# Kernel optimization log

Measured on AMD Instinct MI355X. Metric: run time of the kernel, lower is better.

## Reference

```python
import jax, jax.numpy as jnp
import numpy as np

N_NODES = 100000
N_EDGES = 1600000
IN_F = 128
HID = 128
OUT_F = 40


def _gcn_conv(x, W, b, src, dst):
    # PyG GCNConv: h = x @ W; out[dst] += norm * h[src]; out += b
    n = x.shape[0]
    h = x @ W  # [N, out_channels]
    deg = jnp.zeros((n,), h.dtype).at[dst].add(jnp.ones((dst.shape[0],), h.dtype))
    dinv = jnp.where(deg > 0, jax.lax.rsqrt(deg), 0.0)  # deg^{-1/2}
    norm = dinv[src] * dinv[dst]  # [E+N]
    msg = h[src] * norm[:, None]  # [E+N, out_channels] gather
    out = jnp.zeros_like(h).at[dst].add(msg)  # scatter-add at targets
    if b is not None:
        out = out + b
    return out


def setup_inputs() -> dict:
    key = jax.random.key(0)
    k_x, k_e, k1, k2, k3, kb1, kb2 = jax.random.split(key, 7)
    x = jax.random.normal(k_x, (N_NODES, IN_F), dtype=jnp.float32)
    edge_index = jax.random.randint(k_e, (2, N_EDGES), 0, N_NODES, dtype=jnp.int64)
    s_in = 1.0 / np.sqrt(IN_F)
    s_h = 1.0 / np.sqrt(HID)
    W_in = jax.random.normal(k1, (IN_F, HID), dtype=jnp.float32) * s_in
    b_in = jnp.zeros((HID,), dtype=jnp.float32)
    W_mid = jax.random.normal(k2, (HID, HID), dtype=jnp.float32) * s_h
    b_mid = jnp.zeros((HID,), dtype=jnp.float32)
    W_out = jax.random.normal(k3, (HID, OUT_F), dtype=jnp.float32) * s_h
    return {"x": x, "edge_index": edge_index, "W_in": W_in, "b_in": b_in,
            "W_mid": W_mid, "b_mid": b_mid, "W_out": W_out}


def reference(x, edge_index, W_in, b_in, W_mid, b_mid, W_out):
    n = x.shape[0]
    loops = jnp.arange(n, dtype=edge_index.dtype)
    src = jnp.concatenate([edge_index[0], loops])  # add self-loops
    dst = jnp.concatenate([edge_index[1], loops])
    h = jax.nn.relu(_gcn_conv(x, W_in, b_in, src, dst))
    h = jax.nn.relu(_gcn_conv(h, W_mid, b_mid, src, dst))
    h = _gcn_conv(h, W_out, None, src, dst)  # out_conv: bias=False
    return jax.nn.log_softmax(h, axis=1)
```

## Files before the change

kernel.cpp:

```cpp
#include <hip/hip_runtime.h>
#include <math.h>

#define N_NODES 100000
#define N_EDGES 1600000
#define NBUCK 391
#define BSTRIDE 4608

typedef __attribute__((ext_vector_type(8))) _Float16 h8v;
typedef __attribute__((ext_vector_type(4))) float f32x4;


__launch_bounds__(256)
__global__ void k_bpart(const int* __restrict__ srcv, const int* __restrict__ dstv,
                        int* __restrict__ bcnt, unsigned int* __restrict__ ebuf) {
    __shared__ int hist[NBUCK];
    __shared__ int cur[NBUCK];
    const int tid = threadIdx.x;
    for (int t = tid; t < NBUCK; t += 256) hist[t] = 0;
    __syncthreads();
    const int base = blockIdx.x * 4096;
#pragma unroll
    for (int i = 0; i < 16; i++) {
        int e = base + i * 256 + tid;
        if (e < N_EDGES) atomicAdd(&hist[dstv[e] >> 8], 1);
    }
    __syncthreads();
    for (int t = tid; t < NBUCK; t += 256)
        if (hist[t]) cur[t] = t * BSTRIDE + atomicAdd(&bcnt[t], hist[t]);
    __syncthreads();
#pragma unroll
    for (int i = 0; i < 16; i++) {
        int e = base + i * 256 + tid;
        if (e < N_EDGES) {
            int d = dstv[e];
            int p = atomicAdd(&cur[d >> 8], 1);
            ebuf[p] = ((unsigned int)srcv[e] << 8) | (unsigned int)(d & 255);
        }
    }
}

__launch_bounds__(256)
__global__ void k_bucket(const unsigned int* __restrict__ ebuf, const int* __restrict__ bcnt,
                         int2* __restrict__ rowse, float* __restrict__ dinv,
                         int* __restrict__ colidx) {
    __shared__ int cnt[256];
    __shared__ int s[256];
    __shared__ int cur[256];
    const int tid = threadIdx.x;
    const int b = blockIdx.x;
    const int e0 = b * BSTRIDE;
    const int e1 = e0 + bcnt[b];
    cnt[tid] = 0;
    __syncthreads();
    for (int e = e0 + tid; e < e1; e += 256) atomicAdd(&cnt[ebuf[e] & 255u], 1);
    __syncthreads();
    int v = cnt[tid];
    int x = v;
    s[tid] = x;
    __syncthreads();
    for (int d = 1; d < 256; d <<= 1) {
        int t = (tid >= d) ? s[tid - d] : 0;
        __syncthreads();
        x += t;
        s[tid] = x;
        __syncthreads();
    }
    int start = e0 + x - v;
    int node = b * 256 + tid;
    if (node < N_NODES) {
        rowse[node] = make_int2(start, start + v);
        dinv[node] = rsqrtf((float)(v + 1));
    }
    cur[tid] = start;
    __syncthreads();
    for (int e = e0 + tid; e < e1; e += 256) {
        unsigned int sd = ebuf[e];
        int pos = atomicAdd(&cur[sd & 255u], 1);
        colidx[pos] = (int)(sd >> 8);
    }
}

__global__ void k_zrows(_Float16* __restrict__ bufA, _Float16* __restrict__ zbuf) {
    int t = threadIdx.x;
    if (t < 128) bufA[(size_t)N_NODES * 128 + t] = (_Float16)0.f;
    if (t < 64)  zbuf[(size_t)N_NODES * 64 + t] = (_Float16)0.f;
}


__global__ void k_wprep_all(const float* __restrict__ W1, const float* __restrict__ W2,
                            const float* __restrict__ W3, _Float16* __restrict__ Wt) {
    int idx = blockIdx.x * blockDim.x + threadIdx.x;
    if (idx >= 304 * 128) return;
    int n = idx / 128, k = idx % 128;
    const float* W;
    int ncols, nloc;
    _Float16 *ph, *pl;
    if (n < 128)      { W = W1; ncols = 128; nloc = n;       ph = Wt;                 pl = Wt + 128 * 128; }
    else if (n < 256) { W = W2; ncols = 128; nloc = n - 128; ph = Wt + 2 * 128 * 128; pl = Wt + 3 * 128 * 128; }
    else              { W = W3; ncols = 40;  nloc = n - 256; ph = Wt + 4 * 128 * 128; pl = Wt + 4 * 128 * 128 + 48 * 128; }
    float v = (nloc < ncols) ? W[k * ncols + nloc] : 0.f;
    _Float16 hi = (_Float16)v;
    _Float16 lo = (_Float16)(v - (float)hi);
    ph[nloc * 128 + k] = hi;
    pl[nloc * 128 + k] = lo;
}


#define GEMM_GRID 625
#define NTILES 3125

__launch_bounds__(256, 2)
__global__ void k_gemm128_f32(const float* __restrict__ Af,
                              const _Float16* __restrict__ Wthi, const _Float16* __restrict__ Wtlo,
                              const float* __restrict__ dinv, _Float16* __restrict__ out) {
    const int lane = threadIdx.x & 63;
    const int wi = threadIdx.x >> 6;
    const int nb = wi * 32;
    const int nn = lane & 15;
    const int kq = (lane >> 4) * 8;
    const int quad = lane >> 4;

    h8v bh[4][2], bl[4][2];
#pragma unroll
    for (int c = 0; c < 4; c++)
#pragma unroll
        for (int t = 0; t < 2; t++) {
            int off = (nb + t * 16 + nn) * 128 + c * 32 + kq;
            bh[c][t] = *(const h8v*)(Wthi + off);
            bl[c][t] = *(const h8v*)(Wtlo + off);
        }

    for (int rt = blockIdx.x; rt < NTILES; rt += GEMM_GRID) {
        const int r0 = rt * 32;
        f32x4 acc[2][2] = {};
#pragma unroll
        for (int c = 0; c < 4; c++) {
            h8v a[2];
#pragma unroll
            for (int m = 0; m < 2; m++) {
                const float* p = Af + (size_t)(r0 + m * 16 + nn) * 128 + c * 32 + kq;
                float4 p0 = *(const float4*)p;
                float4 p1 = *(const float4*)(p + 4);
                h8v av = {(_Float16)p0.x, (_Float16)p0.y, (_Float16)p0.z, (_Float16)p0.w,
                          (_Float16)p1.x, (_Float16)p1.y, (_Float16)p1.z, (_Float16)p1.w};
                a[m] = av;
            }
#pragma unroll
            for (int m = 0; m < 2; m++)
#pragma unroll
                for (int t = 0; t < 2; t++) {
                    acc[m][t] = __builtin_amdgcn_mfma_f32_16x16x32_f16(a[m], bh[c][t], acc[m][t], 0, 0, 0);
                    acc[m][t] = __builtin_amdgcn_mfma_f32_16x16x32_f16(a[m], bl[c][t], acc[m][t], 0, 0, 0);
                }
        }
#pragma unroll
        for (int m = 0; m < 2; m++)
#pragma unroll
            for (int reg = 0; reg < 4; reg++) {
                int r = r0 + m * 16 + quad * 4 + reg;
                float dv = dinv[r];
#pragma unroll
                for (int t = 0; t < 2; t++)
                    out[(size_t)r * 128 + nb + t * 16 + nn] = (_Float16)(acc[m][t][reg] * dv);
            }
    }
}

__launch_bounds__(256, 2)
__global__ void k_gemm128(const _Float16* __restrict__ A,
                          const _Float16* __restrict__ Wthi, const _Float16* __restrict__ Wtlo,
                          const float* __restrict__ dinv, _Float16* __restrict__ out) {
    const int lane = threadIdx.x & 63;
    const int wi = threadIdx.x >> 6;
    const int nb = wi * 32;
    const int nn = lane & 15;
    const int kq = (lane >> 4) * 8;
    const int quad = lane >> 4;

    h8v bh[4][2], bl[4][2];
#pragma unroll
    for (int c = 0; c < 4; c++)
#pragma unroll
        for (int t = 0; t < 2; t++) {
            int off = (nb + t * 16 + nn) * 128 + c * 32 + kq;
            bh[c][t] = *(const h8v*)(Wthi + off);
            bl[c][t] = *(const h8v*)(Wtlo + off);
        }

    for (int rt = blockIdx.x; rt < NTILES; rt += GEMM_GRID) {
        const int r0 = rt * 32;
        f32x4 acc[2][2] = {};
#pragma unroll
        for (int c = 0; c < 4; c++) {
            h8v a[2];
#pragma unroll
            for (int m = 0; m < 2; m++)
                a[m] = *(const h8v*)(A + (size_t)(r0 + m * 16 + nn) * 128 + c * 32 + kq);
#pragma unroll
            for (int m = 0; m < 2; m++)
#pragma unroll
                for (int t = 0; t < 2; t++) {
                    acc[m][t] = __builtin_amdgcn_mfma_f32_16x16x32_f16(a[m], bh[c][t], acc[m][t], 0, 0, 0);
                    acc[m][t] = __builtin_amdgcn_mfma_f32_16x16x32_f16(a[m], bl[c][t], acc[m][t], 0, 0, 0);
                }
        }
#pragma unroll
        for (int m = 0; m < 2; m++)
#pragma unroll
            for (int reg = 0; reg < 4; reg++) {
                int r = r0 + m * 16 + quad * 4 + reg;
                float dv = dinv[r];
#pragma unroll
                for (int t = 0; t < 2; t++)
                    out[(size_t)r * 128 + nb + t * 16 + nn] = (_Float16)(acc[m][t][reg] * dv);
            }
    }
}

#define G40_GRID 160

__launch_bounds__(256, 2)
__global__ void k_gemm40(const _Float16* __restrict__ A,
                         const _Float16* __restrict__ Wthi, const _Float16* __restrict__ Wtlo,
                         const float* __restrict__ dinv, _Float16* __restrict__ out) {
    const int lane = threadIdx.x & 63;
    const int wi = threadIdx.x >> 6;
    const int nn = lane & 15;
    const int kq = (lane >> 4) * 8;
    const int quad = lane >> 4;

    h8v bh[4][3], bl[4][3];
#pragma unroll
    for (int c = 0; c < 4; c++)
#pragma unroll
        for (int t = 0; t < 3; t++) {
            int off = (t * 16 + nn) * 128 + c * 32 + kq;
            bh[c][t] = *(const h8v*)(Wthi + off);
            bl[c][t] = *(const h8v*)(Wtlo + off);
        }

    for (int rt = blockIdx.x * 4 + wi; rt < NTILES; rt += G40_GRID * 4) {
        const int r0 = rt * 32;
        f32x4 acc[2][3] = {};
#pragma unroll
        for (int c = 0; c < 4; c++) {
            h8v a[2];
#pragma unroll
            for (int m = 0; m < 2; m++)
                a[m] = *(const h8v*)(A + (size_t)(r0 + m * 16 + nn) * 128 + c * 32 + kq);
#pragma unroll
            for (int m = 0; m < 2; m++)
#pragma unroll
                for (int t = 0; t < 3; t++) {
                    acc[m][t] = __builtin_amdgcn_mfma_f32_16x16x32_f16(a[m], bh[c][t], acc[m][t], 0, 0, 0);
                    acc[m][t] = __builtin_amdgcn_mfma_f32_16x16x32_f16(a[m], bl[c][t], acc[m][t], 0, 0, 0);
                }
        }
#pragma unroll
        for (int m = 0; m < 2; m++)
#pragma unroll
            for (int reg = 0; reg < 4; reg++) {
                int r = r0 + m * 16 + quad * 4 + reg;
                float dv = dinv[r];
#pragma unroll
                for (int t = 0; t < 3; t++)
                    out[(size_t)r * 64 + t * 16 + nn] = (_Float16)(acc[m][t][reg] * dv);
            }
    }
}


__launch_bounds__(256)
__global__ void k_agg4(const _Float16* __restrict__ hp, const int2* __restrict__ rowse,
                       const int* __restrict__ colidx, const float* __restrict__ bias,
                       _Float16* __restrict__ outp) {
    const int lane = threadIdx.x & 63;
    const int wid = (blockIdx.x * blockDim.x + threadIdx.x) >> 6;
    const int rs = lane >> 4;
    const int cp = lane & 15;
    const int r = wid * 4 + rs;

    const int2 se = rowse[r];
    const int deg = se.y - se.x;
    int m = deg;
    m = max(m, __shfl_xor(m, 16));
    m = max(m, __shfl_xor(m, 32));

    const _Float16* hpc = hp + cp * 8;
    h8v acc = {};
    for (int it = 0; it < m; it += 4) {
        int i0 = se.x + it;
        int s0 = colidx[i0];
        int s1 = colidx[i0 + 1];
        int s2 = colidx[i0 + 2];
        int s3 = colidx[i0 + 3];
        s0 = (it < deg) ? s0 : N_NODES;
        s1 = (it + 1 < deg) ? s1 : N_NODES;
        s2 = (it + 2 < deg) ? s2 : N_NODES;
        s3 = (it + 3 < deg) ? s3 : N_NODES;
        h8v v0 = *(const h8v*)(hpc + (size_t)s0 * 128);
        h8v v1 = *(const h8v*)(hpc + (size_t)s1 * 128);
        h8v v2 = *(const h8v*)(hpc + (size_t)s2 * 128);
        h8v v3 = *(const h8v*)(hpc + (size_t)s3 * 128);
        acc += v0;
        acc += v1;
        acc += v2;
        acc += v3;
    }

    h8v sv = *(const h8v*)(hpc + (size_t)r * 128);
    float dv = rsqrtf((float)(deg + 1));
    const float* bp = bias + cp * 8;
    float4 b0 = *(const float4*)bp;
    float4 b1 = *(const float4*)(bp + 4);
    float bb[8] = {b0.x, b0.y, b0.z, b0.w, b1.x, b1.y, b1.z, b1.w};
    h8v o;
#pragma unroll
    for (int j = 0; j < 8; j++) {
        float s = (float)acc[j] + (float)sv[j];
        o[j] = (_Float16)fmaxf(fmaf(dv, s, bb[j]), 0.f);
    }
    *(h8v*)(outp + (size_t)r * 128 + cp * 8) = o;
}


__launch_bounds__(256)
__global__ void k_agg_out(const _Float16* __restrict__ hp, const int2* __restrict__ rowse,
                          const int* __restrict__ colidx, float* __restrict__ out) {
    const int lane = threadIdx.x & 63;
    const int wid = (blockIdx.x * blockDim.x + threadIdx.x) >> 6;
    const int rs = lane >> 3;
    const int cp = lane & 7;
    const int r = wid * 8 + rs;

    const int2 se = rowse[r];
    const int deg = se.y - se.x;
    int m = deg;
    m = max(m, __shfl_xor(m, 8));
    m = max(m, __shfl_xor(m, 16));
    m = max(m, __shfl_xor(m, 32));

    const _Float16* hpc = hp + cp * 8;
    h8v acc = {};
    for (int it = 0; it < m; it += 4) {
        int i0 = se.x + it;
        int s0 = colidx[i0];
        int s1 = colidx[i0 + 1];
        int s2 = colidx[i0 + 2];
        int s3 = colidx[i0 + 3];
        s0 = (it < deg) ? s0 : N_NODES;
        s1 = (it + 1 < deg) ? s1 : N_NODES;
        s2 = (it + 2 < deg) ? s2 : N_NODES;
        s3 = (it + 3 < deg) ? s3 : N_NODES;
        h8v v0 = *(const h8v*)(hpc + (size_t)s0 * 64);
        h8v v1 = *(const h8v*)(hpc + (size_t)s1 * 64);
        h8v v2 = *(const h8v*)(hpc + (size_t)s2 * 64);
        h8v v3 = *(const h8v*)(hpc + (size_t)s3 * 64);
        acc += v0;
        acc += v1;
        acc += v2;
        acc += v3;
    }

    h8v sv = *(const h8v*)(hpc + (size_t)r * 64);
    float dv = rsqrtf((float)(deg + 1));
    float z[8];
#pragma unroll
    for (int j = 0; j < 8; j++) z[j] = dv * ((float)acc[j] + (float)sv[j]);

    const bool act = cp < 5;
    float pm = -INFINITY;
    if (act) {
#pragma unroll
        for (int j = 0; j < 8; j++) pm = fmaxf(pm, z[j]);
    }
    pm = fmaxf(pm, __shfl_xor(pm, 1));
    pm = fmaxf(pm, __shfl_xor(pm, 2));
    pm = fmaxf(pm, __shfl_xor(pm, 4));
    float pe = 0.f;
    if (act) {
#pragma unroll
        for (int j = 0; j < 8; j++) pe += __expf(z[j] - pm);
    }
    pe += __shfl_xor(pe, 1);
    pe += __shfl_xor(pe, 2);
    pe += __shfl_xor(pe, 4);
    float lse = __logf(pe);
    if (act) {
        float* po = out + (size_t)r * 40 + cp * 8;
        float4 o0 = make_float4(z[0] - pm - lse, z[1] - pm - lse, z[2] - pm - lse, z[3] - pm - lse);
        float4 o1 = make_float4(z[4] - pm - lse, z[5] - pm - lse, z[6] - pm - lse, z[7] - pm - lse);
        *(float4*)po = o0;
        *(float4*)(po + 4) = o1;
    }
}


extern "C" void kernel_launch(void* const* d_in, const int* in_sizes, int n_in,
                              void* d_out, int out_size, void* d_ws, size_t ws_size,
                              hipStream_t stream) {
    const float* x     = (const float*)d_in[0];
    const int*   ei    = (const int*)d_in[1];
    const float* W_in  = (const float*)d_in[2];
    const float* b_in  = (const float*)d_in[3];
    const float* W_mid = (const float*)d_in[4];
    const float* b_mid = (const float*)d_in[5];
    const float* W_out = (const float*)d_in[6];
    float* out = (float*)d_out;

    const int* srcv = ei;
    const int* dstv = ei + N_EDGES;

    char* w = (char*)d_ws;
    float* dinv   = (float*)(w);
    int2* rowse   = (int2*)(w + (1ull << 19));
    int* bcnt     = (int*)(w + 1507328);
    int* colidx   = (int*)(w + (2ull << 20));
    unsigned int* ebuf = (unsigned int*)(w + (10ull << 20));
    _Float16* Wt  = (_Float16*)(w + (18ull << 20));
    _Float16* bufA = (_Float16*)(w + (19ull << 20));
    _Float16* bufB = (_Float16*)(w + (45ull << 20));
    _Float16* zbuf = (_Float16*)(w + (71ull << 20));

    _Float16* W1h = Wt;
    _Float16* W1l = Wt + 128 * 128;
    _Float16* W2h = Wt + 2 * 128 * 128;
    _Float16* W2l = Wt + 3 * 128 * 128;
    _Float16* W3h = Wt + 4 * 128 * 128;
    _Float16* W3l = Wt + 4 * 128 * 128 + 48 * 128;

    const int NB_PART = (N_EDGES + 4095) / 4096;

    hipMemsetAsync(bcnt, 0, NBUCK * sizeof(int), stream);
    k_zrows<<<1, 256, 0, stream>>>(bufA, zbuf);
    k_bpart<<<NB_PART, 256, 0, stream>>>(srcv, dstv, bcnt, ebuf);
    k_bucket<<<NBUCK, 256, 0, stream>>>(ebuf, bcnt, rowse, dinv, colidx);

    k_wprep_all<<<(304 * 128 + 255) / 256, 256, 0, stream>>>(W_in, W_mid, W_out, Wt);

    const int AGG4_BLOCKS = N_NODES / 16;
    const int AGGO_BLOCKS = N_NODES / 32;

    k_gemm128_f32<<<GEMM_GRID, 256, 0, stream>>>(x, W1h, W1l, dinv, bufA);
    k_agg4<<<AGG4_BLOCKS, 256, 0, stream>>>(bufA, rowse, colidx, b_in, bufB);
    k_gemm128<<<GEMM_GRID, 256, 0, stream>>>(bufB, W2h, W2l, dinv, bufA);
    k_agg4<<<AGG4_BLOCKS, 256, 0, stream>>>(bufA, rowse, colidx, b_mid, bufB);
    k_gemm40<<<G40_GRID, 256, 0, stream>>>(bufB, W3h, W3l, dinv, zbuf);
    k_agg_out<<<AGGO_BLOCKS, 256, 0, stream>>>(zbuf, rowse, colidx, out);
}
```

Baseline: 366.9 us.

## Store hidden features column-blocked so aggregation gathers from cache-resident slices

Hidden feature buffers move from row-major [N,128] to eight column blocks of 16 halves per node, each block laid out as [N+1,16]. The GEMMs read and write in this blocked layout. The 128-wide aggregation kernel now runs one column block per grid slice, so each block's gather touches a 3.2MB slice that can stay in cache instead of the full 25MB table. The cost is that edge indices and row ranges are re-read eight times, and each gather is only 32 bytes per lane pair. Column-index loads are also marked nontemporal.

```diff
diff --git a/kernel.cpp b/kernel.cpp
--- a/kernel.cpp
+++ b/kernel.cpp
@@ -8,6 +8,7 @@
 
 typedef __attribute__((ext_vector_type(8))) _Float16 h8v;
 typedef __attribute__((ext_vector_type(4))) float f32x4;
+
 
 
 __launch_bounds__(256)
@@ -82,7 +83,9 @@
 
 __global__ void k_zrows(_Float16* __restrict__ bufA, _Float16* __restrict__ zbuf) {
     int t = threadIdx.x;
-    if (t < 128) bufA[(size_t)N_NODES * 128 + t] = (_Float16)0.f;
+    if (t < 128) {
+        bufA[((size_t)(t >> 4) * (N_NODES + 1) + N_NODES) * 16 + (t & 15)] = (_Float16)0.f;
+    }
     if (t < 64)  zbuf[(size_t)N_NODES * 64 + t] = (_Float16)0.f;
 }
 
@@ -160,8 +163,10 @@
                 int r = r0 + m * 16 + quad * 4 + reg;
                 float dv = dinv[r];
 #pragma unroll
-                for (int t = 0; t < 2; t++)
-                    out[(size_t)r * 128 + nb + t * 16 + nn] = (_Float16)(acc[m][t][reg] * dv);
+                for (int t = 0; t < 2; t++) {
+                    int blk = (nb >> 4) + t;
+                    out[((size_t)blk * (N_NODES + 1) + r) * 16 + nn] = (_Float16)(acc[m][t][reg] * dv);
+                }
             }
     }
 }
@@ -194,8 +199,10 @@
         for (int c = 0; c < 4; c++) {
             h8v a[2];
 #pragma unroll
-            for (int m = 0; m < 2; m++)
-                a[m] = *(const h8v*)(A + (size_t)(r0 + m * 16 + nn) * 128 + c * 32 + kq);
+            for (int m = 0; m < 2; m++) {
+                int blk = 2 * c + (kq >> 4);
+                a[m] = *(const h8v*)(A + ((size_t)blk * (N_NODES + 1) + (r0 + m * 16 + nn)) * 16 + (kq & 8));
+            }
 #pragma unroll
             for (int m = 0; m < 2; m++)
 #pragma unroll
@@ -211,8 +218,10 @@
                 int r = r0 + m * 16 + quad * 4 + reg;
                 float dv = dinv[r];
 #pragma unroll
-                for (int t = 0; t < 2; t++)
-                    out[(size_t)r * 128 + nb + t * 16 + nn] = (_Float16)(acc[m][t][reg] * dv);
+                for (int t = 0; t < 2; t++) {
+                    int blk = (nb >> 4) + t;
+                    out[((size_t)blk * (N_NODES + 1) + r) * 16 + nn] = (_Float16)(acc[m][t][reg] * dv);
+                }
             }
     }
 }
@@ -246,8 +255,10 @@
         for (int c = 0; c < 4; c++) {
             h8v a[2];
 #pragma unroll
-            for (int m = 0; m < 2; m++)
-                a[m] = *(const h8v*)(A + (size_t)(r0 + m * 16 + nn) * 128 + c * 32 + kq);
+            for (int m = 0; m < 2; m++) {
+                int blk = 2 * c + (kq >> 4);
+                a[m] = *(const h8v*)(A + ((size_t)blk * (N_NODES + 1) + (r0 + m * 16 + nn)) * 16 + (kq & 8));
+            }
 #pragma unroll
             for (int m = 0; m < 2; m++)
 #pragma unroll
@@ -275,52 +286,60 @@
                        const int* __restrict__ colidx, const float* __restrict__ bias,
                        _Float16* __restrict__ outp) {
     const int lane = threadIdx.x & 63;
-    const int wid = (blockIdx.x * blockDim.x + threadIdx.x) >> 6;
-    const int rs = lane >> 4;
-    const int cp = lane & 15;
-    const int r = wid * 4 + rs;
-
-    const int2 se = rowse[r];
+    const int wi = threadIdx.x >> 6;
+    const int c = blockIdx.x & 7;
+    const int tile = blockIdx.x >> 3;
+    const int rs = lane >> 1;
+    const int cp = lane & 1;
+    const int r = tile * 128 + wi * 32 + rs;
+
+    int2 se = make_int2(0, 0);
+    if (r < N_NODES) se = rowse[r];
     const int deg = se.y - se.x;
     int m = deg;
+    m = max(m, __shfl_xor(m, 2));
+    m = max(m, __shfl_xor(m, 4));
+    m = max(m, __shfl_xor(m, 8));
     m = max(m, __shfl_xor(m, 16));
     m = max(m, __shfl_xor(m, 32));
 
-    const _Float16* hpc = hp + cp * 8;
+    const _Float16* hpc = hp + ((size_t)c * (N_NODES + 1)) * 16 + cp * 8;
     h8v acc = {};
     for (int it = 0; it < m; it += 4) {
         int i0 = se.x + it;
-        int s0 = colidx[i0];
-        int s1 = colidx[i0 + 1];
-        int s2 = colidx[i0 + 2];
-        int s3 = colidx[i0 + 3];
+        int s0 = __builtin_nontemporal_load(colidx + i0);
+        int s1 = __builtin_nontemporal_load(colidx + i0 + 1);
+        int s2 = __builtin_nontemporal_load(colidx + i0 + 2);
+        int s3 = __builtin_nontemporal_load(colidx + i0 + 3);
         s0 = (it < deg) ? s0 : N_NODES;
         s1 = (it + 1 < deg) ? s1 : N_NODES;
         s2 = (it + 2 < deg) ? s2 : N_NODES;
         s3 = (it + 3 < deg) ? s3 : N_NODES;
-        h8v v0 = *(const h8v*)(hpc + (size_t)s0 * 128);
-        h8v v1 = *(const h8v*)(hpc + (size_t)s1 * 128);
-        h8v v2 = *(const h8v*)(hpc + (size_t)s2 * 128);
-        h8v v3 = *(const h8v*)(hpc + (size_t)s3 * 128);
+        h8v v0 = *(const h8v*)(hpc + (size_t)s0 * 16);
+        h8v v1 = *(const h8v*)(hpc + (size_t)s1 * 16);
+        h8v v2 = *(const h8v*)(hpc + (size_t)s2 * 16);
+        h8v v3 = *(const h8v*)(hpc + (size_t)s3 * 16);
         acc += v0;
         acc += v1;
         acc += v2;
         acc += v3;
     }
 
-    h8v sv = *(const h8v*)(hpc + (size_t)r * 128);
-    float dv = rsqrtf((float)(deg + 1));
-    const float* bp = bias + cp * 8;
-    float4 b0 = *(const float4*)bp;
-    float4 b1 = *(const float4*)(bp + 4);
-    float bb[8] = {b0.x, b0.y, b0.z, b0.w, b1.x, b1.y, b1.z, b1.w};
-    h8v o;
-#pragma unroll
-    for (int j = 0; j < 8; j++) {
-        float s = (float)acc[j] + (float)sv[j];
-        o[j] = (_Float16)fmaxf(fmaf(dv, s, bb[j]), 0.f);
-    }
-    *(h8v*)(outp + (size_t)r * 128 + cp * 8) = o;
+    if (r < N_NODES) {
+        h8v sv = *(const h8v*)(hpc + (size_t)r * 16);
+        float dv = rsqrtf((float)(deg + 1));
+        const float* bp = bias + c * 16 + cp * 8;
+        float4 b0 = *(const float4*)bp;
+        float4 b1 = *(const float4*)(bp + 4);
+        float bb[8] = {b0.x, b0.y, b0.z, b0.w, b1.x, b1.y, b1.z, b1.w};
+        h8v o;
+#pragma unroll
+        for (int j = 0; j < 8; j++) {
+            float sx = (float)acc[j] + (float)sv[j];
+            o[j] = (_Float16)fmaxf(fmaf(dv, sx, bb[j]), 0.f);
+        }
+        *(h8v*)(outp + ((size_t)c * (N_NODES + 1) + r) * 16 + cp * 8) = o;
+    }
 }
 
 
@@ -438,7 +457,7 @@
 
     k_wprep_all<<<(304 * 128 + 255) / 256, 256, 0, stream>>>(W_in, W_mid, W_out, Wt);
 
-    const int AGG4_BLOCKS = N_NODES / 16;
+    const int AGG4_BLOCKS = 8 * ((N_NODES + 127) / 128);
     const int AGGO_BLOCKS = N_NODES / 32;
 
     k_gemm128_f32<<<GEMM_GRID, 256, 0, stream>>>(x, W1h, W1l, dinv, bufA);
```

New measurement: 505.4 us. 37.7% more time.

## Fuse first GEMM, edge partition and weight prep into one prep kernel

Applied to the files above, without the earlier changes.

Merges the first-layer GEMM (x@W1), the edge bucket partition, the W2/W3 fp16 split prep and the zero-row init into a single heterogeneous launch, with the GEMM converting W1 on the fly. Because the GEMM no longer waits for dinv, the dinv row scaling moves into k_bucket, which rescales bufA in place after building the CSR. This removes several launches and lets the dense GEMM overlap with the irregular partition work. In exchange bufA is read and written an extra time, and each GEMM block recomputes the W1 hi/lo split from strided global reads.

```diff
diff --git a/kernel.cpp b/kernel.cpp
--- a/kernel.cpp
+++ b/kernel.cpp
@@ -8,17 +8,115 @@
 
 typedef __attribute__((ext_vector_type(8))) _Float16 h8v;
 typedef __attribute__((ext_vector_type(4))) float f32x4;
-
-
-__launch_bounds__(256)
-__global__ void k_bpart(const int* __restrict__ srcv, const int* __restrict__ dstv,
-                        int* __restrict__ bcnt, unsigned int* __restrict__ ebuf) {
+typedef __attribute__((ext_vector_type(2))) int i32x2;
+
+#define GEMM_GRID 625
+#define NTILES 3125
+
+
+__global__ void k_prep(const int* __restrict__ srcv, const int* __restrict__ dstv,
+                       int* __restrict__ bcnt, unsigned int* __restrict__ ebuf,
+                       const float* __restrict__ x, const float* __restrict__ W1,
+                       const float* __restrict__ W2, const float* __restrict__ W3,
+                       _Float16* __restrict__ Wt,
+                       _Float16* __restrict__ bufA, _Float16* __restrict__ bufB,
+                       _Float16* __restrict__ zbuf) {
+    const int tid = threadIdx.x;
+    const int bid = blockIdx.x;
+
+    if (bid < 625) {
+        const int lane = tid & 63;
+        const int wi = tid >> 6;
+        const int nb = wi * 32;
+        const int nn = lane & 15;
+        const int quad = lane >> 4;
+        const int kq = quad * 8;
+
+        h8v bh[4][2], bl[4][2];
+#pragma unroll
+        for (int c = 0; c < 4; c++)
+#pragma unroll
+            for (int t = 0; t < 2; t++) {
+#pragma unroll
+                for (int j = 0; j < 8; j++) {
+                    float w = W1[(c * 32 + kq + j) * 128 + nb + t * 16 + nn];
+                    _Float16 hi = (_Float16)w;
+                    bh[c][t][j] = hi;
+                    bl[c][t][j] = (_Float16)(w - (float)hi);
+                }
+            }
+
+        for (int rt = bid; rt < NTILES; rt += GEMM_GRID) {
+            const int r0 = rt * 32;
+            f32x4 acc[2][2] = {};
+#pragma unroll
+            for (int c = 0; c < 4; c++) {
+                h8v a[2];
+#pragma unroll
+                for (int m = 0; m < 2; m++) {
+                    const float* p = x + (size_t)(r0 + m * 16 + nn) * 128 + c * 32 + kq;
+                    float4 p0 = *(const float4*)p;
+                    float4 p1 = *(const float4*)(p + 4);
+                    h8v av = {(_Float16)p0.x, (_Float16)p0.y, (_Float16)p0.z, (_Float16)p0.w,
+                              (_Float16)p1.x, (_Float16)p1.y, (_Float16)p1.z, (_Float16)p1.w};
+                    a[m] = av;
+                }
+#pragma unroll
+                for (int m = 0; m < 2; m++)
+#pragma unroll
+                    for (int t = 0; t < 2; t++) {
+                        acc[m][t] = __builtin_amdgcn_mfma_f32_16x16x32_f16(a[m], bh[c][t], acc[m][t], 0, 0, 0);
+                        acc[m][t] = __builtin_amdgcn_mfma_f32_16x16x32_f16(a[m], bl[c][t], acc[m][t], 0, 0, 0);
+                    }
+            }
+#pragma unroll
+            for (int m = 0; m < 2; m++)
+#pragma unroll
+                for (int reg = 0; reg < 4; reg++) {
+                    int r = r0 + m * 16 + quad * 4 + reg;
+#pragma unroll
+                    for (int t = 0; t < 2; t++)
+                        bufA[(size_t)r * 128 + nb + t * 16 + nn] = (_Float16)acc[m][t][reg];
+                }
+        }
+        return;
+    }
+
+    if (bid >= 1016) {
+        if (bid == 1104) {
+            if (tid < 128) {
+                bufA[(size_t)N_NODES * 128 + tid] = (_Float16)0.f;
+                bufB[(size_t)N_NODES * 128 + tid] = (_Float16)0.f;
+            }
+            if (tid < 64)  zbuf[(size_t)N_NODES * 64 + tid] = (_Float16)0.f;
+            return;
+        }
+        int idx = (bid - 1016) * 256 + tid;
+        if (idx >= 176 * 128) return;
+        int n = idx / 128, k = idx % 128;
+        _Float16 *ph, *pl;
+        float v;
+        if (n < 128) {
+            v = W2[k * 128 + n];
+            ph = Wt + 2 * 128 * 128; pl = Wt + 3 * 128 * 128;
+        } else {
+            int nloc = n - 128;
+            v = (nloc < 40) ? W3[k * 40 + nloc] : 0.f;
+            ph = Wt + 4 * 128 * 128; pl = Wt + 4 * 128 * 128 + 48 * 128;
+            n = nloc;
+        }
+        _Float16 hi = (_Float16)v;
+        _Float16 lo = (_Float16)(v - (float)hi);
+        ph[n * 128 + k] = hi;
+        pl[n * 128 + k] = lo;
+        return;
+    }
+
     __shared__ int hist[NBUCK];
     __shared__ int cur[NBUCK];
-    const int tid = threadIdx.x;
     for (int t = tid; t < NBUCK; t += 256) hist[t] = 0;
     __syncthreads();
-    const int base = blockIdx.x * 4096;
+    const int base = (bid - 625) * 4096;
 #pragma unroll
     for (int i = 0; i < 16; i++) {
         int e = base + i * 256 + tid;
@@ -39,13 +137,15 @@
     }
 }
 
+
 __launch_bounds__(256)
 __global__ void k_bucket(const unsigned int* __restrict__ ebuf, const int* __restrict__ bcnt,
-                         int2* __restrict__ rowse, float* __restrict__ dinv,
-                         int* __restrict__ colidx) {
+                         i32x2* __restrict__ rowse, float* __restrict__ dinv,
+                         int* __restrict__ colidx, _Float16* __restrict__ bufA) {
     __shared__ int cnt[256];
     __shared__ int s[256];
     __shared__ int cur[256];
+    __shared__ float sdv[256];
     const int tid = threadIdx.x;
     const int b = blockIdx.x;
     const int e0 = b * BSTRIDE;
@@ -67,9 +167,14 @@
     }
     int start = e0 + x - v;
     int node = b * 256 + tid;
+    float dvv = rsqrtf((float)(v + 1));
+    sdv[tid] = dvv;
     if (node < N_NODES) {
-        rowse[node] = make_int2(start, start + v);
-        dinv[node] = rsqrtf((float)(v + 1));
+        i32x2 se;
+        se.x = start;
+        se.y = start + v;
+        rowse[node] = se;
+        dinv[node] = dvv;
     }
     cur[tid] = start;
     __syncthreads();
@@ -78,200 +183,28 @@
         int pos = atomicAdd(&cur[sd & 255u], 1);
         colidx[pos] = (int)(sd >> 8);
     }
-}
-
-__global__ void k_zrows(_Float16* __restrict__ bufA, _Float16* __restrict__ zbuf) {
-    int t = threadIdx.x;
-    if (t < 128) bufA[(size_t)N_NODES * 128 + t] = (_Float16)0.f;
-    if (t < 64)  zbuf[(size_t)N_NODES * 64 + t] = (_Float16)0.f;
-}
-
-
-__global__ void k_wprep_all(const float* __restrict__ W1, const float* __restrict__ W2,
-                            const float* __restrict__ W3, _Float16* __restrict__ Wt) {
-    int idx = blockIdx.x * blockDim.x + threadIdx.x;
-    if (idx >= 304 * 128) return;
-    int n = idx / 128, k = idx % 128;
-    const float* W;
-    int ncols, nloc;
-    _Float16 *ph, *pl;
-    if (n < 128)      { W = W1; ncols = 128; nloc = n;       ph = Wt;                 pl = Wt + 128 * 128; }
-    else if (n < 256) { W = W2; ncols = 128; nloc = n - 128; ph = Wt + 2 * 128 * 128; pl = Wt + 3 * 128 * 128; }
-    else              { W = W3; ncols = 40;  nloc = n - 256; ph = Wt + 4 * 128 * 128; pl = Wt + 4 * 128 * 128 + 48 * 128; }
-    float v = (nloc < ncols) ? W[k * ncols + nloc] : 0.f;
-    _Float16 hi = (_Float16)v;
-    _Float16 lo = (_Float16)(v - (float)hi);
-    ph[nloc * 128 + k] = hi;
-    pl[nloc * 128 + k] = lo;
-}
-
-
-#define GEMM_GRID 625
-#define NTILES 3125
-
-__launch_bounds__(256, 2)
-__global__ void k_gemm128_f32(const float* __restrict__ Af,
-                              const _Float16* __restrict__ Wthi, const _Float16* __restrict__ Wtlo,
-                              const float* __restrict__ dinv, _Float16* __restrict__ out) {
-    const int lane = threadIdx.x & 63;
-    const int wi = threadIdx.x >> 6;
-    const int nb = wi * 32;
-    const int nn = lane & 15;
-    const int kq = (lane >> 4) * 8;
-    const int quad = lane >> 4;
-
-    h8v bh[4][2], bl[4][2];
-#pragma unroll
-    for (int c = 0; c < 4; c++)
-#pragma unroll
-        for (int t = 0; t < 2; t++) {
-            int off = (nb + t * 16 + nn) * 128 + c * 32 + kq;
-            bh[c][t] = *(const h8v*)(Wthi + off);
-            bl[c][t] = *(const h8v*)(Wtlo + off);
-        }
-
-    for (int rt = blockIdx.x; rt < NTILES; rt += GEMM_GRID) {
-        const int r0 = rt * 32;
-        f32x4 acc[2][2] = {};
-#pragma unroll
-        for (int c = 0; c < 4; c++) {
-            h8v a[2];
-#pragma unroll
-            for (int m = 0; m < 2; m++) {
-                const float* p = Af + (size_t)(r0 + m * 16 + nn) * 128 + c * 32 + kq;
-                float4 p0 = *(const float4*)p;
-                float4 p1 = *(const float4*)(p + 4);
-                h8v av = {(_Float16)p0.x, (_Float16)p0.y, (_Float16)p0.z, (_Float16)p0.w,
-                          (_Float16)p1.x, (_Float16)p1.y, (_Float16)p1.z, (_Float16)p1.w};
-                a[m] = av;
-            }
-#pragma unroll
-            for (int m = 0; m < 2; m++)
-#pragma unroll
-                for (int t = 0; t < 2; t++) {
-                    acc[m][t] = __builtin_amdgcn_mfma_f32_16x16x32_f16(a[m], bh[c][t], acc[m][t], 0, 0, 0);
-                    acc[m][t] = __builtin_amdgcn_mfma_f32_16x16x32_f16(a[m], bl[c][t], acc[m][t], 0, 0, 0);
-                }
-        }
-#pragma unroll
-        for (int m = 0; m < 2; m++)
-#pragma unroll
-            for (int reg = 0; reg < 4; reg++) {
-                int r = r0 + m * 16 + quad * 4 + reg;
-                float dv = dinv[r];
-#pragma unroll
-                for (int t = 0; t < 2; t++)
-                    out[(size_t)r * 128 + nb + t * 16 + nn] = (_Float16)(acc[m][t][reg] * dv);
-            }
-    }
-}
-
-__launch_bounds__(256, 2)
-__global__ void k_gemm128(const _Float16* __restrict__ A,
-                          const _Float16* __restrict__ Wthi, const _Float16* __restrict__ Wtlo,
-                          const float* __restrict__ dinv, _Float16* __restrict__ out) {
-    const int lane = threadIdx.x & 63;
-    const int wi = threadIdx.x >> 6;
-    const int nb = wi * 32;
-    const int nn = lane & 15;
-    const int kq = (lane >> 4) * 8;
-    const int quad = lane >> 4;
-
-    h8v bh[4][2], bl[4][2];
-#pragma unroll
-    for (int c = 0; c < 4; c++)
-#pragma unroll
-        for (int t = 0; t < 2; t++) {
-            int off = (nb + t * 16 + nn) * 128 + c * 32 + kq;
-            bh[c][t] = *(const h8v*)(Wthi + off);
-            bl[c][t] = *(const h8v*)(Wtlo + off);
-        }
-
-    for (int rt = blockIdx.x; rt < NTILES; rt += GEMM_GRID) {
-        const int r0 = rt * 32;
-        f32x4 acc[2][2] = {};
-#pragma unroll
-        for (int c = 0; c < 4; c++) {
-            h8v a[2];
-#pragma unroll
-            for (int m = 0; m < 2; m++)
-                a[m] = *(const h8v*)(A + (size_t)(r0 + m * 16 + nn) * 128 + c * 32 + kq);
-#pragma unroll
-            for (int m = 0; m < 2; m++)
-#pragma unroll
-                for (int t = 0; t < 2; t++) {
-                    acc[m][t] = __builtin_amdgcn_mfma_f32_16x16x32_f16(a[m], bh[c][t], acc[m][t], 0, 0, 0);
-                    acc[m][t] = __builtin_amdgcn_mfma_f32_16x16x32_f16(a[m], bl[c][t], acc[m][t], 0, 0, 0);
-                }
-        }
-#pragma unroll
-        for (int m = 0; m < 2; m++)
-#pragma unroll
-            for (int reg = 0; reg < 4; reg++) {
-                int r = r0 + m * 16 + quad * 4 + reg;
-                float dv = dinv[r];
-#pragma unroll
-                for (int t = 0; t < 2; t++)
-                    out[(size_t)r * 128 + nb + t * 16 + nn] = (_Float16)(acc[m][t][reg] * dv);
-            }
-    }
-}
-
-#define G40_GRID 160
-
-__launch_bounds__(256, 2)
-__global__ void k_gemm40(const _Float16* __restrict__ A,
-                         const _Float16* __restrict__ Wthi, const _Float16* __restrict__ Wtlo,
-                         const float* __restrict__ dinv, _Float16* __restrict__ out) {
-    const int lane = threadIdx.x & 63;
-    const int wi = threadIdx.x >> 6;
-    const int nn = lane & 15;
-    const int kq = (lane >> 4) * 8;
-    const int quad = lane >> 4;
-
-    h8v bh[4][3], bl[4][3];
-#pragma unroll
-    for (int c = 0; c < 4; c++)
-#pragma unroll
-        for (int t = 0; t < 3; t++) {
-            int off = (t * 16 + nn) * 128 + c * 32 + kq;
-            bh[c][t] = *(const h8v*)(Wthi + off);
-            bl[c][t] = *(const h8v*)(Wtlo + off);
-        }
-
-    for (int rt = blockIdx.x * 4 + wi; rt < NTILES; rt += G40_GRID * 4) {
-        const int r0 = rt * 32;
-        f32x4 acc[2][3] = {};
-#pragma unroll
-        for (int c = 0; c < 4; c++) {
-            h8v a[2];
-#pragma unroll
-            for (int m = 0; m < 2; m++)
-                a[m] = *(const h8v*)(A + (size_t)(r0 + m * 16 + nn) * 128 + c * 32 + kq);
-#pragma unroll
-            for (int m = 0; m < 2; m++)
-#pragma unroll
-                for (int t = 0; t < 3; t++) {
-                    acc[m][t] = __builtin_amdgcn_mfma_f32_16x16x32_f16(a[m], bh[c][t], acc[m][t], 0, 0, 0);
-                    acc[m][t] = __builtin_amdgcn_mfma_f32_16x16x32_f16(a[m], bl[c][t], acc[m][t], 0, 0, 0);
-                }
-        }
-#pragma unroll
-        for (int m = 0; m < 2; m++)
-#pragma unroll
-            for (int reg = 0; reg < 4; reg++) {
-                int r = r0 + m * 16 + quad * 4 + reg;
-                float dv = dinv[r];
-#pragma unroll
-                for (int t = 0; t < 3; t++)
-                    out[(size_t)r * 64 + t * 16 + nn] = (_Float16)(acc[m][t][reg] * dv);
-            }
+    __syncthreads();
+    const int b0row = b * 256;
+    const int chunk = tid & 15;
+#pragma unroll
+    for (int i = 0; i < 16; i++) {
+        int rl = i * 16 + (tid >> 4);
+        int row = b0row + rl;
+        if (row < N_NODES) {
+            _Float16* p = bufA + (size_t)row * 128 + chunk * 8;
+            h8v vv = *(const h8v*)p;
+            float d = sdv[rl];
+            h8v o;
+#pragma unroll
+            for (int j = 0; j < 8; j++) o[j] = (_Float16)(d * (float)vv[j]);
+            *(h8v*)p = o;
+        }
     }
 }
 
 
 __launch_bounds__(256)
-__global__ void k_agg4(const _Float16* __restrict__ hp, const int2* __restrict__ rowse,
+__global__ void k_agg4(const _Float16* __restrict__ hp, const i32x2* __restrict__ rowse,
                        const int* __restrict__ colidx, const float* __restrict__ bias,
                        _Float16* __restrict__ outp) {
     const int lane = threadIdx.x & 63;
@@ -280,7 +213,7 @@
     const int cp = lane & 15;
     const int r = wid * 4 + rs;
 
-    const int2 se = rowse[r];
+    const i32x2 se = rowse[r];
     const int deg = se.y - se.x;
     int m = deg;
     m = max(m, __shfl_xor(m, 16));
@@ -324,8 +257,112 @@
 }
 
 
+__launch_bounds__(256, 2)
+__global__ void k_gemm128(const _Float16* __restrict__ A,
+                          const _Float16* __restrict__ Wthi, const _Float16* __restrict__ Wtlo,
+                          const float* __restrict__ dinv, _Float16* __restrict__ out) {
+    const int lane = threadIdx.x & 63;
+    const int wi = threadIdx.x >> 6;
+    const int nb = wi * 32;
+    const int nn = lane & 15;
+    const int kq = (lane >> 4) * 8;
+    const int quad = lane >> 4;
+
+    h8v bh[4][2], bl[4][2];
+#pragma unroll
+    for (int c = 0; c < 4; c++)
+#pragma unroll
+        for (int t = 0; t < 2; t++) {
+            int off = (nb + t * 16 + nn) * 128 + c * 32 + kq;
+            bh[c][t] = *(const h8v*)(Wthi + off);
+            bl[c][t] = *(const h8v*)(Wtlo + off);
+        }
+
+    for (int rt = blockIdx.x; rt < NTILES; rt += GEMM_GRID) {
+        const int r0 = rt * 32;
+        f32x4 acc[2][2] = {};
+#pragma unroll
+        for (int c = 0; c < 4; c++) {
+            h8v a[2];
+#pragma unroll
+            for (int m = 0; m < 2; m++)
+                a[m] = *(const h8v*)(A + (size_t)(r0 + m * 16 + nn) * 128 + c * 32 + kq);
+#pragma unroll
+            for (int m = 0; m < 2; m++)
+#pragma unroll
+                for (int t = 0; t < 2; t++) {
+                    acc[m][t] = __builtin_amdgcn_mfma_f32_16x16x32_f16(a[m], bh[c][t], acc[m][t], 0, 0, 0);
+                    acc[m][t] = __builtin_amdgcn_mfma_f32_16x16x32_f16(a[m], bl[c][t], acc[m][t], 0, 0, 0);
+                }
+        }
+#pragma unroll
+        for (int m = 0; m < 2; m++)
+#pragma unroll
+            for (int reg = 0; reg < 4; reg++) {
+                int r = r0 + m * 16 + quad * 4 + reg;
+                float dv = dinv[r];
+#pragma unroll
+                for (int t = 0; t < 2; t++)
+                    out[(size_t)r * 128 + nb + t * 16 + nn] = (_Float16)(acc[m][t][reg] * dv);
+            }
+    }
+}
+
+#define G40_GRID 160
+
+__launch_bounds__(256, 2)
+__global__ void k_gemm40(const _Float16* __restrict__ A,
+                         const _Float16* __restrict__ Wthi, const _Float16* __restrict__ Wtlo,
+                         const float* __restrict__ dinv, _Float16* __restrict__ out) {
+    const int lane = threadIdx.x & 63;
+    const int wi = threadIdx.x >> 6;
+    const int nn = lane & 15;
+    const int kq = (lane >> 4) * 8;
+    const int quad = lane >> 4;
+
+    h8v bh[4][3], bl[4][3];
+#pragma unroll
+    for (int c = 0; c < 4; c++)
+#pragma unroll
+        for (int t = 0; t < 3; t++) {
+            int off = (t * 16 + nn) * 128 + c * 32 + kq;
+            bh[c][t] = *(const h8v*)(Wthi + off);
+            bl[c][t] = *(const h8v*)(Wtlo + off);
+        }
+
+    for (int rt = blockIdx.x * 4 + wi; rt < NTILES; rt += G40_GRID * 4) {
+        const int r0 = rt * 32;
+        f32x4 acc[2][3] = {};
+#pragma unroll
+        for (int c = 0; c < 4; c++) {
+            h8v a[2];
+#pragma unroll
+            for (int m = 0; m < 2; m++)
+                a[m] = *(const h8v*)(A + (size_t)(r0 + m * 16 + nn) * 128 + c * 32 + kq);
+#pragma unroll
+            for (int m = 0; m < 2; m++)
+#pragma unroll
+                for (int t = 0; t < 3; t++) {
+                    acc[m][t] = __builtin_amdgcn_mfma_f32_16x16x32_f16(a[m], bh[c][t], acc[m][t], 0, 0, 0);
+                    acc[m][t] = __builtin_amdgcn_mfma_f32_16x16x32_f16(a[m], bl[c][t], acc[m][t], 0, 0, 0);
+                }
+        }
+#pragma unroll
+        for (int m = 0; m < 2; m++)
+#pragma unroll
+            for (int reg = 0; reg < 4; reg++) {
+                int r = r0 + m * 16 + quad * 4 + reg;
+                float dv = dinv[r];
+#pragma unroll
+                for (int t = 0; t < 3; t++)
+                    out[(size_t)r * 64 + t * 16 + nn] = (_Float16)(acc[m][t][reg] * dv);
+            }
+    }
+}
+
+
 __launch_bounds__(256)
-__global__ void k_agg_out(const _Float16* __restrict__ hp, const int2* __restrict__ rowse,
+__global__ void k_agg_out(const _Float16* __restrict__ hp, const i32x2* __restrict__ rowse,
                           const int* __restrict__ colidx, float* __restrict__ out) {
     const int lane = threadIdx.x & 63;
     const int wid = (blockIdx.x * blockDim.x + threadIdx.x) >> 6;
@@ -333,7 +370,7 @@
     const int cp = lane & 7;
     const int r = wid * 8 + rs;
 
-    const int2 se = rowse[r];
+    const i32x2 se = rowse[r];
     const int deg = se.y - se.x;
     int m = deg;
     m = max(m, __shfl_xor(m, 8));
@@ -413,7 +450,7 @@
 
     char* w = (char*)d_ws;
     float* dinv   = (float*)(w);
-    int2* rowse   = (int2*)(w + (1ull << 19));
+    i32x2* rowse  = (i32x2*)(w + (1ull << 19));
     int* bcnt     = (int*)(w + 1507328);
     int* colidx   = (int*)(w + (2ull << 20));
     unsigned int* ebuf = (unsigned int*)(w + (10ull << 20));
@@ -422,26 +459,19 @@
     _Float16* bufB = (_Float16*)(w + (45ull << 20));
     _Float16* zbuf = (_Float16*)(w + (71ull << 20));
 
-    _Float16* W1h = Wt;
-    _Float16* W1l = Wt + 128 * 128;
     _Float16* W2h = Wt + 2 * 128 * 128;
     _Float16* W2l = Wt + 3 * 128 * 128;
     _Float16* W3h = Wt + 4 * 128 * 128;
     _Float16* W3l = Wt + 4 * 128 * 128 + 48 * 128;
 
-    const int NB_PART = (N_EDGES + 4095) / 4096;
-
-    hipMemsetAsync(bcnt, 0, NBUCK * sizeof(int), stream);
-    k_zrows<<<1, 256, 0, stream>>>(bufA, zbuf);
-    k_bpart<<<NB_PART, 256, 0, stream>>>(srcv, dstv, bcnt, ebuf);
-    k_bucket<<<NBUCK, 256, 0, stream>>>(ebuf, bcnt, rowse, dinv, colidx);
-
-    k_wprep_all<<<(304 * 128 + 255) / 256, 256, 0, stream>>>(W_in, W_mid, W_out, Wt);
+    (void)hipMemsetAsync(bcnt, 0, NBUCK * sizeof(int), stream);
+    k_prep<<<1105, 256, 0, stream>>>(srcv, dstv, bcnt, ebuf, x, W_in, W_mid, W_out,
+                                     Wt, bufA, bufB, zbuf);
+    k_bucket<<<NBUCK, 256, 0, stream>>>(ebuf, bcnt, rowse, dinv, colidx, bufA);
 
     const int AGG4_BLOCKS = N_NODES / 16;
     const int AGGO_BLOCKS = N_NODES / 32;
 
-    k_gemm128_f32<<<GEMM_GRID, 256, 0, stream>>>(x, W1h, W1l, dinv, bufA);
     k_agg4<<<AGG4_BLOCKS, 256, 0, stream>>>(bufA, rowse, colidx, b_in, bufB);
     k_gemm128<<<GEMM_GRID, 256, 0, stream>>>(bufB, W2h, W2l, dinv, bufA);
     k_agg4<<<AGG4_BLOCKS, 256, 0, stream>>>(bufA, rowse, colidx, b_mid, bufB);
```

Result: no change. 363.0 us (-1.1%).
